# Performance work log

Hardware: AMD Instinct MI355X
Metric: run time of the kernel (lower is better)

Reference implementation:

```python
import jax, jax.numpy as jnp
import numpy as np

THRESH = 0.3
EPS = 1e-8
M = 256
D = 768


def setup_inputs() -> dict:
    key = jax.random.key(0)
    kx, kb, ka, kn = jax.random.split(key, 4)
    x = jax.random.normal(kx, (1, D), dtype=jnp.float32)
    base = jax.random.normal(kb, (M, D), dtype=jnp.float32)
    # correlate memories with x so that a realistic fraction passes the 0.3 cosine threshold
    alpha = jax.random.uniform(ka, (M,), minval=0.0, maxval=0.8)
    mem = alpha[:, None] * x[0][None, :] + jnp.sqrt(1.0 - alpha**2)[:, None] * base
    # pre-sampled injection noise (original: torch.randn * 0.1 per W element)
    noise = 0.1 * jax.random.normal(kn, (M, M, D), dtype=jnp.float32)
    return {"x": x, "mem": mem, "noise": noise}


def reference(x, mem, noise):
    # x: [1, D] query embedding; mem: [M, D] memory bank (k == memory embeddings)
    d = x.shape[-1]
    xv = x[0]                                   # [D]
    nx = jnp.maximum(jnp.linalg.norm(xv), EPS)
    nm = jnp.linalg.norm(mem, axis=-1)          # [M]
    nm_s = jnp.maximum(nm, EPS)
    Sx = xv.sum()
    Sm = mem.sum(-1)                            # [M]

    kx_dot = mem @ xv                           # [M] dot(k_i, x)
    mx_cos = kx_dot / (nm_s * nx)               # [M] cos(x, m_j) == cos(k_i, x)
    mask = (mx_cos > THRESH).astype(x.dtype)    # active memories A
    cnt = mask.sum()

    km_dot = mem @ mem.T                        # [M, M] dot(k_i, m_j)
    km_cos = km_dot / (nm_s[:, None] * nm_s[None, :])

    # c[a, i] = cos(k_i, m_a) + cos(k_i, x)  (scalar added to all D dims of k_i)
    c = km_cos.T + mx_cos[None, :]              # [M, M]

    # ||k'_{a,i}||^2 = ||k_i||^2 + 2 c sum(k_i) + D c^2
    nkp = jnp.sqrt(jnp.maximum(nm[None, :]**2 + 2.0 * c * Sm[None, :] + d * c**2, EPS**2))

    # cos(k'_{a,i}, x) = (dot(k_i,x) + c*sum(x)) / (||k'|| * ||x||)
    cos_kp_x = (kx_dot[None, :] + c * Sx) / (nkp * nx)

    # mean over a' in A of cos(k'_{a,i}, m_{a'}) in closed form
    A1 = (km_dot * (mask / nm_s)[None, :]).sum(-1)   # [M] (i-indexed)
    A2 = ((mask * Sm) / nm_s).sum()                  # scalar
    denom = nkp * jnp.maximum(cnt, 1.0)
    mean_cos_km = jnp.where(cnt > 0, (A1[None, :] + c * A2) / denom, 0.0)

    # W_{a,i} = k'_{a,i} + mean sim to x + mean sim to active mems; then noise; O_prev = 0
    W = mem[None, :, :] + (c + cos_kp_x + mean_cos_km)[:, :, None]   # [M, M, D]
    out = (W + noise) * mask[:, None, None]     # zero rows for inactive memories
    return out
```

## Files before the change

kernel.cpp:

```cpp
#include <hip/hip_runtime.h>
#include <hip/hip_bf16.h>
#include <math.h>

#define M 256
#define D 768
#define D4 (D/4)
#define THRESH 0.3
#define EPS 1e-8

#define WS_SM    0
#define WS_NM2   256
#define WS_KX    512
#define WS_NMS   768
#define WS_MX    1024
#define WS_W     1280
#define WS_A1    1536
#define WS_MASK  1792
#define WS_V     2048
#define WS_SX    2816
#define WS_NX2   2817
#define WS_NX    2818
#define WS_CNT   2819
#define WS_A2    2820
#define WS_S     3072

__global__ void row_stats_kernel(const float* __restrict__ x,
                                 const float* __restrict__ mem,
                                 float* __restrict__ ws) {
    const int r = blockIdx.x;
    const int t = threadIdx.x;
    const float* row = (r < M) ? (mem + (size_t)r * D) : x;

    double s = 0.0, sq = 0.0, dt = 0.0;
    for (int d = t; d < D; d += 256) {
        double m = (double)row[d];
        double xv = (double)x[d];
        s += m; sq += m * m; dt += m * xv;
    }
    __shared__ double sh0[256], sh1[256], sh2[256];
    sh0[t] = s; sh1[t] = sq; sh2[t] = dt;
    __syncthreads();
    for (int k = 128; k > 0; k >>= 1) {
        if (t < k) { sh0[t] += sh0[t + k]; sh1[t] += sh1[t + k]; sh2[t] += sh2[t + k]; }
        __syncthreads();
    }
    if (t == 0) {
        if (r < M) {
            ws[WS_SM + r]  = (float)sh0[0];
            ws[WS_NM2 + r] = (float)sh1[0];
            ws[WS_KX + r]  = (float)sh2[0];
        } else {
            ws[WS_SX]  = (float)sh0[0];
            ws[WS_NX2] = (float)sh1[0];
        }
    }
}

__global__ void stats2_kernel(float* __restrict__ ws) {
    const int i = threadIdx.x;
    double nx = sqrt(fmax((double)ws[WS_NX2], 0.0));
    nx = fmax(nx, EPS);
    double nm2 = (double)ws[WS_NM2 + i];
    double nm  = sqrt(fmax(nm2, 0.0));
    double nms = fmax(nm, EPS);
    double mx  = (double)ws[WS_KX + i] / (nms * nx);
    double mask = (mx > THRESH) ? 1.0 : 0.0;
    double w = mask / nms;

    ws[WS_NMS + i]  = (float)nms;
    ws[WS_MX + i]   = (float)mx;
    ws[WS_W + i]    = (float)w;
    ws[WS_MASK + i] = (float)mask;

    __shared__ double shc[256], sha[256];
    shc[i] = mask;
    sha[i] = mask * (double)ws[WS_SM + i] / nms;
    __syncthreads();
    for (int k = 128; k > 0; k >>= 1) {
        if (i < k) { shc[i] += shc[i + k]; sha[i] += sha[i + k]; }
        __syncthreads();
    }
    if (i == 0) {
        ws[WS_NX]  = (float)nx;
        ws[WS_CNT] = (float)shc[0];
        ws[WS_A2]  = (float)sha[0];
    }
}

__global__ void compute_v_kernel(const float* __restrict__ mem, float* __restrict__ ws) {
    const int d = blockIdx.x * 256 + threadIdx.x;
    __shared__ float wsh[M];
    if (threadIdx.x < M) wsh[threadIdx.x] = ws[WS_W + threadIdx.x];
    __syncthreads();
    double acc = 0.0;
    for (int j = 0; j < M; ++j)
        acc += (double)wsh[j] * (double)mem[(size_t)j * D + d];
    ws[WS_V + d] = (float)acc;
}

__global__ void compute_A1_kernel(const float* __restrict__ mem, float* __restrict__ ws) {
    const int i = blockIdx.x, t = threadIdx.x;
    double acc = 0.0;
    for (int d = t; d < D; d += 256)
        acc += (double)mem[(size_t)i * D + d] * (double)ws[WS_V + d];
    __shared__ double sh[256];
    sh[t] = acc;
    __syncthreads();
    for (int k = 128; k > 0; k >>= 1) {
        if (t < k) sh[t] += sh[t + k];
        __syncthreads();
    }
    if (t == 0) ws[WS_A1 + i] = (float)sh[0];
}

__global__ void compute_s_kernel(const float* __restrict__ mem, float* __restrict__ ws) {
    const int a = blockIdx.x, i = threadIdx.x;
    __shared__ float4 arow[D4];
    if (i < D4) arow[i] = ((const float4*)(mem + (size_t)a * D))[i];
    __syncthreads();

    const float4* rowi = (const float4*)(mem + (size_t)i * D);
    double km = 0.0;
    for (int d = 0; d < D4; ++d) {
        float4 m = rowi[d];
        float4 av = arow[d];
        km += (double)m.x * av.x + (double)m.y * av.y
            + (double)m.z * av.z + (double)m.w * av.w;
    }
    double nmsa = (double)ws[WS_NMS + a];
    double nmsi = (double)ws[WS_NMS + i];
    double c = km / (nmsa * nmsi) + (double)ws[WS_MX + i];

    double nm2 = (double)ws[WS_NM2 + i];
    double Sm  = (double)ws[WS_SM + i];
    double kx  = (double)ws[WS_KX + i];
    double nkp = sqrt(fmax(nm2 + 2.0 * c * Sm + (double)D * c * c, EPS * EPS));

    double nx  = (double)ws[WS_NX];
    double Sx  = (double)ws[WS_SX];
    double cos_kp_x = (kx + c * Sx) / (nkp * nx);

    double cnt = (double)ws[WS_CNT];
    double A2  = (double)ws[WS_A2];
    double A1  = (double)ws[WS_A1 + i];
    double mean_cos_km = (cnt > 0.0) ? (A1 + c * A2) / (nkp * fmax(cnt, 1.0)) : 0.0;

    ws[WS_S + a * M + i] = (float)(c + cos_kp_x + mean_cos_km);
}

__global__ __launch_bounds__(D4) void final_kernel(const float* __restrict__ mem,
                                                   const float* __restrict__ noise,
                                                   const float* __restrict__ ws,
                                                   float* __restrict__ out) {
    const int i = blockIdx.x;
    const int a = blockIdx.y;
    const int t = threadIdx.x;
    const size_t idx = ((size_t)(a * M + i)) * D4 + t;

    float4 o;
    if (ws[WS_MASK + a] != 0.0f) {
        const float s = ws[WS_S + a * M + i];
        float4 m = ((const float4*)mem)[(size_t)i * D4 + t];
        float4 n = ((const float4*)noise)[idx];
        o.x = m.x + s + n.x;
        o.y = m.y + s + n.y;
        o.z = m.z + s + n.z;
        o.w = m.w + s + n.w;
    } else {
        o = make_float4(0.f, 0.f, 0.f, 0.f);
    }
    ((float4*)out)[idx] = o;
}

extern "C" void kernel_launch(void* const* d_in, const int* in_sizes, int n_in,
                              void* d_out, int out_size, void* d_ws, size_t ws_size,
                              hipStream_t stream) {
    const float* x     = (const float*)d_in[0];
    const float* mem   = (const float*)d_in[1];
    const float* noise = (const float*)d_in[2];
    float* out = (float*)d_out;
    float* ws  = (float*)d_ws;

    row_stats_kernel<<<dim3(M + 1), dim3(256), 0, stream>>>(x, mem, ws);
    stats2_kernel<<<dim3(1), dim3(256), 0, stream>>>(ws);
    compute_v_kernel<<<dim3(3), dim3(256), 0, stream>>>(mem, ws);
    compute_A1_kernel<<<dim3(M), dim3(256), 0, stream>>>(mem, ws);
    compute_s_kernel<<<dim3(M), dim3(256), 0, stream>>>(mem, ws);
    final_kernel<<<dim3(M, M), dim3(D4), 0, stream>>>(mem, noise, ws, out);
}
```

Baseline: 372.4 us.

## Fuse A1 and Gram computation via transposed memory; nontemporal final stream

Row-stats kernel now also writes a transposed copy of mem to the workspace. The separate v and A1 kernels are folded into the score kernel, which computes the Gram column with coalesced fp32 accumulation and reduces A1 in shared memory. The Gram dot product drops from double to float. The final elementwise kernel uses nontemporal loads and stores for noise and output, and the score matrix is stored transposed. This cuts two launches and the costly fp64 Gram loop, at the cost of slightly different rounding.

```diff
diff --git a/kernel.cpp b/kernel.cpp
--- a/kernel.cpp
+++ b/kernel.cpp
@@ -8,34 +8,37 @@
 #define THRESH 0.3
 #define EPS 1e-8
 
+typedef float vfloat4 __attribute__((ext_vector_type(4)));
+
 #define WS_SM    0
 #define WS_NM2   256
 #define WS_KX    512
 #define WS_NMS   768
 #define WS_MX    1024
 #define WS_W     1280
-#define WS_A1    1536
-#define WS_MASK  1792
-#define WS_V     2048
-#define WS_SX    2816
-#define WS_NX2   2817
-#define WS_NX    2818
-#define WS_CNT   2819
-#define WS_A2    2820
-#define WS_S     3072
+#define WS_MASK  1536
+#define WS_SX    1792
+#define WS_NX2   1793
+#define WS_NX    1794
+#define WS_CNT   1795
+#define WS_A2    1796
+#define WS_MEMT  2048
+#define WS_ST    (2048 + D * M)
 
-__global__ void row_stats_kernel(const float* __restrict__ x,
-                                 const float* __restrict__ mem,
-                                 float* __restrict__ ws) {
+__global__ void k1_stats_transpose(const float* __restrict__ x,
+                                   const float* __restrict__ mem,
+                                   float* __restrict__ ws) {
     const int r = blockIdx.x;
     const int t = threadIdx.x;
     const float* row = (r < M) ? (mem + (size_t)r * D) : x;
 
     double s = 0.0, sq = 0.0, dt = 0.0;
     for (int d = t; d < D; d += 256) {
-        double m = (double)row[d];
+        float mf = row[d];
+        double m = (double)mf;
         double xv = (double)x[d];
         s += m; sq += m * m; dt += m * xv;
+        if (r < M) ws[WS_MEMT + d * M + r] = mf;
     }
     __shared__ double sh0[256], sh1[256], sh2[256];
     sh0[t] = s; sh1[t] = sq; sh2[t] = dt;
@@ -56,7 +59,7 @@
     }
 }
 
-__global__ void stats2_kernel(float* __restrict__ ws) {
+__global__ void k2_derived(float* __restrict__ ws) {
     const int i = threadIdx.x;
     double nx = sqrt(fmax((double)ws[WS_NX2], 0.0));
     nx = fmax(nx, EPS);
@@ -65,11 +68,10 @@
     double nms = fmax(nm, EPS);
     double mx  = (double)ws[WS_KX + i] / (nms * nx);
     double mask = (mx > THRESH) ? 1.0 : 0.0;
-    double w = mask / nms;
 
     ws[WS_NMS + i]  = (float)nms;
     ws[WS_MX + i]   = (float)mx;
-    ws[WS_W + i]    = (float)w;
+    ws[WS_W + i]    = (float)(mask / nms);
     ws[WS_MASK + i] = (float)mask;
 
     __shared__ double shc[256], sha[256];
@@ -87,89 +89,77 @@
     }
 }
 
-__global__ void compute_v_kernel(const float* __restrict__ mem, float* __restrict__ ws) {
-    const int d = blockIdx.x * 256 + threadIdx.x;
-    __shared__ float wsh[M];
-    if (threadIdx.x < M) wsh[threadIdx.x] = ws[WS_W + threadIdx.x];
+__global__ __launch_bounds__(256) void k3_s(const float* __restrict__ mem,
+                                            float* __restrict__ ws) {
+    const int i = blockIdx.x;
+    const int a = threadIdx.x;
+
+    __shared__ float lrow[D];
+    for (int d = a; d < D; d += 256) lrow[d] = mem[(size_t)i * D + d];
     __syncthreads();
-    double acc = 0.0;
-    for (int j = 0; j < M; ++j)
-        acc += (double)wsh[j] * (double)mem[(size_t)j * D + d];
-    ws[WS_V + d] = (float)acc;
+
+    const float* memT = ws + WS_MEMT;
+    float acc0 = 0.f, acc1 = 0.f, acc2 = 0.f, acc3 = 0.f;
+    #pragma unroll 4
+    for (int d = 0; d < D; d += 4) {
+        acc0 += memT[(d + 0) * M + a] * lrow[d + 0];
+        acc1 += memT[(d + 1) * M + a] * lrow[d + 1];
+        acc2 += memT[(d + 2) * M + a] * lrow[d + 2];
+        acc3 += memT[(d + 3) * M + a] * lrow[d + 3];
+    }
+    const double g = (double)((acc0 + acc1) + (acc2 + acc3));
+
+    __shared__ double shr[256];
+    shr[a] = (double)ws[WS_W + a] * g;
+    __syncthreads();
+    for (int k = 128; k > 0; k >>= 1) {
+        if (a < k) shr[a] += shr[a + k];
+        __syncthreads();
+    }
+    const double A1 = shr[0];
+
+    const double nmsi = (double)ws[WS_NMS + i];
+    const double nm2  = (double)ws[WS_NM2 + i];
+    const double Sm   = (double)ws[WS_SM + i];
+    const double kx   = (double)ws[WS_KX + i];
+    const double mxi  = (double)ws[WS_MX + i];
+    const double nx   = (double)ws[WS_NX];
+    const double Sx   = (double)ws[WS_SX];
+    const double cnt  = (double)ws[WS_CNT];
+    const double A2   = (double)ws[WS_A2];
+
+    const double nmsa = (double)ws[WS_NMS + a];
+    const double c = g / (nmsa * nmsi) + mxi;
+
+    const double nkp = sqrt(fmax(nm2 + 2.0 * c * Sm + (double)D * c * c, EPS * EPS));
+    const double cos_kp_x = (kx + c * Sx) / (nkp * nx);
+    const double mean_cos_km = (cnt > 0.0) ? (A1 + c * A2) / (nkp * fmax(cnt, 1.0)) : 0.0;
+
+    ws[WS_ST + i * M + a] = (float)(c + cos_kp_x + mean_cos_km);
 }
 
-__global__ void compute_A1_kernel(const float* __restrict__ mem, float* __restrict__ ws) {
-    const int i = blockIdx.x, t = threadIdx.x;
-    double acc = 0.0;
-    for (int d = t; d < D; d += 256)
-        acc += (double)mem[(size_t)i * D + d] * (double)ws[WS_V + d];
-    __shared__ double sh[256];
-    sh[t] = acc;
-    __syncthreads();
-    for (int k = 128; k > 0; k >>= 1) {
-        if (t < k) sh[t] += sh[t + k];
-        __syncthreads();
-    }
-    if (t == 0) ws[WS_A1 + i] = (float)sh[0];
-}
-
-__global__ void compute_s_kernel(const float* __restrict__ mem, float* __restrict__ ws) {
-    const int a = blockIdx.x, i = threadIdx.x;
-    __shared__ float4 arow[D4];
-    if (i < D4) arow[i] = ((const float4*)(mem + (size_t)a * D))[i];
-    __syncthreads();
-
-    const float4* rowi = (const float4*)(mem + (size_t)i * D);
-    double km = 0.0;
-    for (int d = 0; d < D4; ++d) {
-        float4 m = rowi[d];
-        float4 av = arow[d];
-        km += (double)m.x * av.x + (double)m.y * av.y
-            + (double)m.z * av.z + (double)m.w * av.w;
-    }
-    double nmsa = (double)ws[WS_NMS + a];
-    double nmsi = (double)ws[WS_NMS + i];
-    double c = km / (nmsa * nmsi) + (double)ws[WS_MX + i];
-
-    double nm2 = (double)ws[WS_NM2 + i];
-    double Sm  = (double)ws[WS_SM + i];
-    double kx  = (double)ws[WS_KX + i];
-    double nkp = sqrt(fmax(nm2 + 2.0 * c * Sm + (double)D * c * c, EPS * EPS));
-
-    double nx  = (double)ws[WS_NX];
-    double Sx  = (double)ws[WS_SX];
-    double cos_kp_x = (kx + c * Sx) / (nkp * nx);
-
-    double cnt = (double)ws[WS_CNT];
-    double A2  = (double)ws[WS_A2];
-    double A1  = (double)ws[WS_A1 + i];
-    double mean_cos_km = (cnt > 0.0) ? (A1 + c * A2) / (nkp * fmax(cnt, 1.0)) : 0.0;
-
-    ws[WS_S + a * M + i] = (float)(c + cos_kp_x + mean_cos_km);
-}
-
-__global__ __launch_bounds__(D4) void final_kernel(const float* __restrict__ mem,
-                                                   const float* __restrict__ noise,
-                                                   const float* __restrict__ ws,
-                                                   float* __restrict__ out) {
+__global__ __launch_bounds__(D4) void k4_final(const float* __restrict__ mem,
+                                               const float* __restrict__ noise,
+                                               const float* __restrict__ ws,
+                                               float* __restrict__ out) {
     const int i = blockIdx.x;
     const int a = blockIdx.y;
     const int t = threadIdx.x;
     const size_t idx = ((size_t)(a * M + i)) * D4 + t;
 
-    float4 o;
+    vfloat4 o;
     if (ws[WS_MASK + a] != 0.0f) {
-        const float s = ws[WS_S + a * M + i];
-        float4 m = ((const float4*)mem)[(size_t)i * D4 + t];
-        float4 n = ((const float4*)noise)[idx];
+        const float s = ws[WS_ST + i * M + a];
+        vfloat4 m = ((const vfloat4*)mem)[(size_t)i * D4 + t];
+        vfloat4 n = __builtin_nontemporal_load((const vfloat4*)noise + idx);
         o.x = m.x + s + n.x;
         o.y = m.y + s + n.y;
         o.z = m.z + s + n.z;
         o.w = m.w + s + n.w;
     } else {
-        o = make_float4(0.f, 0.f, 0.f, 0.f);
+        o = (vfloat4){0.f, 0.f, 0.f, 0.f};
     }
-    ((float4*)out)[idx] = o;
+    __builtin_nontemporal_store(o, (vfloat4*)out + idx);
 }
 
 extern "C" void kernel_launch(void* const* d_in, const int* in_sizes, int n_in,
@@ -181,10 +171,8 @@
     float* out = (float*)d_out;
     float* ws  = (float*)d_ws;
 
-    row_stats_kernel<<<dim3(M + 1), dim3(256), 0, stream>>>(x, mem, ws);
-    stats2_kernel<<<dim3(1), dim3(256), 0, stream>>>(ws);
-    compute_v_kernel<<<dim3(3), dim3(256), 0, stream>>>(mem, ws);
-    compute_A1_kernel<<<dim3(M), dim3(256), 0, stream>>>(mem, ws);
-    compute_s_kernel<<<dim3(M), dim3(256), 0, stream>>>(mem, ws);
-    final_kernel<<<dim3(M, M), dim3(D4), 0, stream>>>(mem, noise, ws, out);
+    k1_stats_transpose<<<dim3(M + 1), dim3(256), 0, stream>>>(x, mem, ws);
+    k2_derived<<<dim3(1), dim3(256), 0, stream>>>(ws);
+    k3_s<<<dim3(M), dim3(256), 0, stream>>>(mem, ws);
+    k4_final<<<dim3(M, M), dim3(D4), 0, stream>>>(mem, noise, ws, out);
 }
```

After: 338.3 us. 1.1x faster.
